# Kernel optimization log

Hardware: AMD Instinct MI355X
Metric: run time of the kernel (lower is better)

The kernel has to match this reference:

```python
import jax, jax.numpy as jnp
import numpy as np

N_NODES = 50000
N_EDGES = 1600000
F_IN = 512      # 2 * embedding_dimension
HID = 512
OUT = 4
NEG_SLOPE = 0.01  # torch LeakyReLU default


def _leaky_relu(x):
    return jnp.where(x >= 0, x, NEG_SLOPE * x)


def setup_inputs() -> dict:
    key = jax.random.key(0)
    ks = jax.random.split(key, 12)
    s_in = 1.0 / np.sqrt(F_IN)
    s_h = 1.0 / np.sqrt(HID)
    return {
        "feature": jax.random.normal(ks[0], (N_NODES, F_IN), jnp.float32),
        "edge_index": jax.random.randint(ks[1], (2, N_EDGES), 0, N_NODES, jnp.int64),
        "edge_type": jax.random.randint(ks[2], (N_EDGES,), 0, 2, jnp.int64),
        # input MLP
        "W_in": jax.random.uniform(ks[3], (F_IN, HID), jnp.float32, -s_in, s_in),
        "b_in": jnp.zeros((HID,), jnp.float32),
        # sage1: lin_l (bias) on aggregated neighbors, lin_r (no bias) on self
        "W1_l": jax.random.uniform(ks[4], (HID, HID), jnp.float32, -s_h, s_h),
        "b1_l": jnp.zeros((HID,), jnp.float32),
        "W1_r": jax.random.uniform(ks[5], (HID, HID), jnp.float32, -s_h, s_h),
        # sage2
        "W2_l": jax.random.uniform(ks[6], (HID, HID), jnp.float32, -s_h, s_h),
        "b2_l": jnp.zeros((HID,), jnp.float32),
        "W2_r": jax.random.uniform(ks[7], (HID, HID), jnp.float32, -s_h, s_h),
        # output linear (hidden -> 4); note forward skips linear_relu_output1
        "W_out": jax.random.uniform(ks[8], (HID, OUT), jnp.float32, -s_h, s_h),
        "b_out": jnp.zeros((OUT,), jnp.float32),
    }


def _sage_conv(x, src, dst, W_l, b_l, W_r):
    # mean aggregation of source features onto destinations (PyG default flow)
    agg = jax.ops.segment_sum(x[src], dst, num_segments=N_NODES)  # [N, H]
    cnt = jax.ops.segment_sum(jnp.ones((src.shape[0], 1), x.dtype), dst,
                              num_segments=N_NODES)               # [N, 1]
    mean = agg / jnp.maximum(cnt, 1.0)
    return mean @ W_l + b_l + x @ W_r


def reference(feature, edge_index, edge_type,
              W_in, b_in, W1_l, b1_l, W1_r, W2_l, b2_l, W2_r, W_out, b_out):
    src, dst = edge_index[0], edge_index[1]
    x = _leaky_relu(feature.astype(jnp.float32) @ W_in + b_in)
    x = _sage_conv(x, src, dst, W1_l, b1_l, W1_r)
    # dropout is identity in eval mode
    x = _sage_conv(x, src, dst, W2_l, b2_l, W2_r)
    return x @ W_out + b_out
```

## Files before the change

kernel.cpp:

```cpp
#include <hip/hip_runtime.h>
#include <stdint.h>

#define NNODES 50000
#define NEDGES 1600000
#define HID 512
#define NEG_SLOPE 0.01f
#define NBUCK 98
#define NBLK 200
#define TILE 8000
#define NSUB 8
#define GPBLK 391
#define MROWS 50048

#define ZTOT4 263040
#define ZBLK 1028
#define TCBLK 1024
#define CABLK 12512
#define SABLK 1025
#define PREP_TC (ZBLK)
#define PREP_CA (ZBLK + TCBLK)
#define PREP_SA (ZBLK + TCBLK + CABLK)
#define PREP_HK (ZBLK + TCBLK + CABLK + SABLK)
#define PREP_GRID (PREP_HK + NBLK)

typedef __attribute__((ext_vector_type(8))) short bf16x8;
typedef __attribute__((ext_vector_type(8))) unsigned short u16x8;
typedef __attribute__((ext_vector_type(4))) float f32x4;

__device__ __forceinline__ unsigned short f2bf(float f) {
  unsigned int u = __builtin_bit_cast(unsigned int, f);
  u += 0x7FFFu + ((u >> 16) & 1u);
  return (unsigned short)(u >> 16);
}
__device__ __forceinline__ void gload_lds16(const void* g, void* l) {
  __builtin_amdgcn_global_load_lds(
      (const __attribute__((address_space(1))) void*)g,
      (__attribute__((address_space(3))) void*)l, 16, 0, 0);
}

__device__ __forceinline__ float wave_dot(const float* __restrict__ Arow,
                                          const float* __restrict__ B, int j) {
  int l = threadIdx.x & 63;
  float4 a0 = *reinterpret_cast<const float4*>(Arow + l * 8);
  float4 a1 = *reinterpret_cast<const float4*>(Arow + l * 8 + 4);
  const float* bb = B + (size_t)(l * 8) * 4 + j;
  float s = a0.x * bb[0] + a0.y * bb[4] + a0.z * bb[8] + a0.w * bb[12] +
            a1.x * bb[16] + a1.y * bb[20] + a1.z * bb[24] + a1.w * bb[28];
#pragma unroll
  for (int off = 1; off < 64; off <<= 1) s += __shfl_xor(s, off);
  return s;
}

__global__ __launch_bounds__(256) void prep(
    const float* __restrict__ feat, const float* __restrict__ W_in,
    const float* __restrict__ W2l, const float* __restrict__ W2r,
    const float* __restrict__ Wout, const float* __restrict__ b2l,
    const float* __restrict__ bout, const int* __restrict__ ei,
    float* __restrict__ zbase, unsigned short* __restrict__ Wt0,
    unsigned short* __restrict__ featb,
    float* __restrict__ Wlp, float* __restrict__ Wrp, float* __restrict__ bp,
    int* __restrict__ hist) {
  __shared__ int h[NBUCK];
  __shared__ int flg;
  int blk = blockIdx.x, t = threadIdx.x;
  if (blk < PREP_TC) {
    int idx = blk * 256 + t;
    if (idx < ZTOT4) reinterpret_cast<float4*>(zbase)[idx] = {0.f, 0.f, 0.f, 0.f};
  } else if (blk < PREP_CA) {
    int i = (blk - PREP_TC) * 256 + t;
    int n = i >> 9, k = i & 511;
    Wt0[i] = f2bf(W_in[(k << 9) | n]);
  } else if (blk < PREP_SA) {
    int idx = (blk - PREP_CA) * 256 + t;
    size_t g = (size_t)idx * 8;
    int row = idx >> 6;
    u16x8 pk;
    if (row < NNODES) {
      float4 v0 = *reinterpret_cast<const float4*>(feat + g);
      float4 v1 = *reinterpret_cast<const float4*>(feat + g + 4);
      pk[0] = f2bf(v0.x); pk[1] = f2bf(v0.y); pk[2] = f2bf(v0.z); pk[3] = f2bf(v0.w);
      pk[4] = f2bf(v1.x); pk[5] = f2bf(v1.y); pk[6] = f2bf(v1.z); pk[7] = f2bf(v1.w);
    } else {
      pk = (u16x8)0;
    }
    *reinterpret_cast<u16x8*>(featb + g) = pk;
  } else if (blk < PREP_HK) {
    int gw = (blk - PREP_SA) * 4 + (t >> 6);
    int l = t & 63;
    if (gw < 2048) {
      float v = wave_dot(W2l + (size_t)(gw >> 2) * 512, Wout, gw & 3);
      if (l == 0) Wlp[gw] = v;
    } else if (gw < 4096) {
      int g = gw - 2048;
      float v = wave_dot(W2r + (size_t)(g >> 2) * 512, Wout, g & 3);
      if (l == 0) Wrp[g] = v;
    } else if (gw < 4100) {
      int j = gw - 4096;
      float v = wave_dot(b2l, Wout, j);
      if (l == 0) bp[j] = v + bout[j];
    }
  } else {
    int hb = blk - PREP_HK;
    for (int i = t; i < NBUCK; i += 256) h[i] = 0;
    if (t < 64) {
      unsigned long long m = __ballot(ei[2 * t + 1] != 0);
      if (t == 0) flg = (m != 0ULL) ? 1 : 0;
    }
    __syncthreads();
    int f = flg;
    int e0 = hb * TILE;
    for (int e = e0 + 2 * t; e < e0 + TILE; e += 512) {
      int d0, d1;
      if (f) {
        int2 v = *reinterpret_cast<const int2*>(&ei[(size_t)NEDGES + e]);
        d0 = v.x; d1 = v.y;
      } else {
        int4 v = *reinterpret_cast<const int4*>(&ei[2 * ((size_t)NEDGES + e)]);
        d0 = v.x; d1 = v.z;
      }
      if ((unsigned)d0 < NNODES) atomicAdd(&h[d0 >> 9], 1);
      if ((unsigned)d1 < NNODES) atomicAdd(&h[d1 >> 9], 1);
    }
    __syncthreads();
    for (int i = t; i < NBUCK; i += 256) hist[i * NBLK + hb] = h[i];
  }
}

__global__ __launch_bounds__(256) void smallB(
    const float* __restrict__ W1l, const float* __restrict__ W1r,
    const float* __restrict__ b1l,
    const float* __restrict__ Wlp, const float* __restrict__ Wrp,
    const float* __restrict__ bp,
    float* __restrict__ Pall, float* __restrict__ kb, float* __restrict__ kc) {
  int gw = blockIdx.x * 4 + (threadIdx.x >> 6);
  int l = threadIdx.x & 63;
  if (gw < 6144) {
    int k = gw / 12, jg = gw % 12;
    int g = jg >> 2, j = jg & 3;
    float v;
    if (g == 0) v = wave_dot(W1l + (size_t)k * 512, Wlp, j);
    else if (g == 1) v = wave_dot(W1r + (size_t)k * 512, Wlp, j) +
                         wave_dot(W1l + (size_t)k * 512, Wrp, j);
    else v = wave_dot(W1r + (size_t)k * 512, Wrp, j);
    if (l == 0) Pall[k * 12 + jg] = v;
  } else if (gw < 6152) {
    int i = gw - 6144, j = i & 3;
    if (i < 4) {
      float v = wave_dot(b1l, Wlp, j);
      if (l == 0) kb[j] = v;
    } else {
      float v = wave_dot(b1l, Wrp, j);
      if (l == 0) kc[j] = v + bp[j];
    }
  }
}

__global__ __launch_bounds__(512) void scanh(int* __restrict__ hist,
                                             int* __restrict__ bstart) {
  __shared__ int s[512];
  const int TOT = NBUCK * NBLK;
  const int C = 40;
  int t = threadIdx.x;
  int base = t * C;
  int sum = 0;
#pragma unroll
  for (int i = 0; i < C; i++) {
    int idx = base + i;
    sum += (idx < TOT) ? hist[idx] : 0;
  }
  s[t] = sum;
  __syncthreads();
  for (int off = 1; off < 512; off <<= 1) {
    int u = (t >= off) ? s[t - off] : 0;
    __syncthreads();
    s[t] += u;
    __syncthreads();
  }
  int run = (t > 0) ? s[t - 1] : 0;
#pragma unroll
  for (int i = 0; i < C; i++) {
    int idx = base + i;
    if (idx < TOT) {
      int v = hist[idx];
      hist[idx] = run;
      if (idx % NBLK == 0) bstart[idx / NBLK] = run;
      run += v;
    }
  }
  if (t == 511) bstart[NBUCK] = s[511];
}

__global__ __launch_bounds__(256) void binscatter(const int* __restrict__ ei,
                                                  const int* __restrict__ hbase,
                                                  unsigned int* __restrict__ pcol) {
  __shared__ unsigned int vals[TILE];
  __shared__ unsigned char bid[TILE];
  __shared__ int lcnt[NBUCK];
  __shared__ int lbase[NBUCK];
  __shared__ int delta[NBUCK];
  __shared__ int flg;
  int t = threadIdx.x, blk = blockIdx.x;
  for (int i = t; i < NBUCK; i += 256) lcnt[i] = 0;
  if (t < 64) {
    unsigned long long m = __ballot(ei[2 * t + 1] != 0);
    if (t == 0) flg = (m != 0ULL) ? 1 : 0;
  }
  __syncthreads();
  int f = flg;
  int e0 = blk * TILE;
  for (int e = e0 + 2 * t; e < e0 + TILE; e += 512) {
    int d0, d1;
    if (f) {
      int2 vd = *reinterpret_cast<const int2*>(&ei[(size_t)NEDGES + e]);
      d0 = vd.x; d1 = vd.y;
    } else {
      int4 vd = *reinterpret_cast<const int4*>(&ei[2 * ((size_t)NEDGES + e)]);
      d0 = vd.x; d1 = vd.z;
    }
    if ((unsigned)d0 < NNODES) atomicAdd(&lcnt[d0 >> 9], 1);
    if ((unsigned)d1 < NNODES) atomicAdd(&lcnt[d1 >> 9], 1);
  }
  __syncthreads();
  if (t == 0) {
    int run = 0;
    for (int b = 0; b < NBUCK; b++) { lbase[b] = run; run += lcnt[b]; }
  }
  __syncthreads();
  for (int b = t; b < NBUCK; b += 256) {
    delta[b] = hbase[b * NBLK + blk] - lbase[b];
    lcnt[b] = 0;
  }
  __syncthreads();
  for (int e = e0 + 2 * t; e < e0 + TILE; e += 512) {
    int s0, s1v, d0, d1;
    if (f) {
      int2 vs = *reinterpret_cast<const int2*>(&ei[e]);
      int2 vd = *reinterpret_cast<const int2*>(&ei[(size_t)NEDGES + e]);
      s0 = vs.x; s1v = vs.y; d0 = vd.x; d1 = vd.y;
    } else {
      int4 vs = *reinterpret_cast<const int4*>(&ei[2 * (size_t)e]);
      int4 vd = *reinterpret_cast<const int4*>(&ei[2 * ((size_t)NEDGES + e)]);
      s0 = vs.x; s1v = vs.z; d0 = vd.x; d1 = vd.z;
    }
    if ((unsigned)d0 < NNODES) {
      if ((unsigned)s0 >= NNODES) s0 = 0;
      int b = d0 >> 9;
      int p = lbase[b] + atomicAdd(&lcnt[b], 1);
      vals[p] = ((unsigned)(d0 & 511) << 16) | (unsigned)s0;
      bid[p] = (unsigned char)b;
    }
    if ((unsigned)d1 < NNODES) {
      if ((unsigned)s1v >= NNODES) s1v = 0;
      int b = d1 >> 9;
      int p = lbase[b] + atomicAdd(&lcnt[b], 1);
      vals[p] = ((unsigned)(d1 & 511) << 16) | (unsigned)s1v;
      bid[p] = (unsigned char)b;
    }
  }
  __syncthreads();
  int total = lbase[NBUCK - 1] + lcnt[NBUCK - 1];
  for (int p = t; p < total; p += 256) {
    pcol[delta[bid[p]] + p] = vals[p];
  }
}

__global__ __launch_bounds__(256, 4) void gemmproj(
    const unsigned short* __restrict__ Ab, const unsigned short* __restrict__ Bt,
    const float* __restrict__ bias, const float* __restrict__ Pall,
    float* __restrict__ t0a, float* __restrict__ t0b, float* __restrict__ t0c) {
  __shared__ unsigned short As[128 * 64];
  __shared__ unsigned short Bs[128 * 64];
  __shared__ float tab[128 * 12];
  const int tid = threadIdx.x;
  const int wave = tid >> 6, lane = tid & 63;
  const int w = blockIdx.x;
  const int mt = (w & 7) + ((w >> 5) << 3);
  const int nb = (w >> 3) & 3;
  if (mt >= GPBLK) return;
  const int bm = mt * 128, bn = nb * 128;
  const int wr = wave >> 1, wc = wave & 1;
  const int r15 = lane & 15, kl = lane >> 4;
  const int srow = lane >> 3;
  const int gslot = (lane & 7) ^ srow;
  const int goff = gslot * 8;

  for (int i = tid; i < 1536; i += 256) tab[i] = 0.f;

  f32x4 acc[4][4];
#pragma unroll
  for (int i = 0; i < 4; i++)
#pragma unroll
    for (int j = 0; j < 4; j++) acc[i][j] = {0.f, 0.f, 0.f, 0.f};

  const int sxa = r15 & 7;

  for (int kt = 0; kt < 8; ++kt) {
#pragma unroll
    for (int q = 0; q < 4; ++q) {
      int c = wave * 4 + q;
      int row = c * 8 + srow;
      gload_lds16(Ab + (size_t)(bm + row) * HID + kt * 64 + goff, (void*)&As[c * 512]);
      gload_lds16(Bt + (size_t)(bn + row) * HID + kt * 64 + goff, (void*)&Bs[c * 512]);
    }
    __syncthreads();
#pragma unroll
    for (int k2 = 0; k2 < 2; ++k2) {
      const int slot = (k2 * 4 + kl) ^ sxa;
      bf16x8 af[4], bfr[4];
#pragma unroll
      for (int mi = 0; mi < 4; ++mi)
        af[mi] = *reinterpret_cast<const bf16x8*>(&As[(wr * 64 + mi * 16 + r15) * 64 + slot * 8]);
#pragma unroll
      for (int ni = 0; ni < 4; ++ni)
        bfr[ni] = *reinterpret_cast<const bf16x8*>(&Bs[(wc * 64 + ni * 16 + r15) * 64 + slot * 8]);
#pragma unroll
      for (int ni = 0; ni < 4; ++ni)
#pragma unroll
        for (int mi = 0; mi < 4; ++mi)
          acc[ni][mi] = __builtin_amdgcn_mfma_f32_16x16x32_bf16(bfr[ni], af[mi], acc[ni][mi], 0, 0, 0);
    }
    __syncthreads();
  }

#pragma unroll
  for (int mi = 0; mi < 4; ++mi) {
    float p12[12];
#pragma unroll
    for (int j = 0; j < 12; ++j) p12[j] = 0.f;
#pragma unroll
    for (int ni = 0; ni < 4; ++ni) {
      int nbase = bn + wc * 64 + ni * 16 + kl * 4;
      float4 bv4 = *reinterpret_cast<const float4*>(bias + nbase);
      float bb[4] = {bv4.x, bv4.y, bv4.z, bv4.w};
#pragma unroll
      for (int rg = 0; rg < 4; ++rg) {
        float v = acc[ni][mi][rg] + bb[rg];
        v = (v >= 0.f) ? v : NEG_SLOPE * v;
        const float* Pc = Pall + (size_t)(nbase + rg) * 12;
        float4 p0 = *reinterpret_cast<const float4*>(Pc);
        float4 p1 = *reinterpret_cast<const float4*>(Pc + 4);
        float4 p2 = *reinterpret_cast<const float4*>(Pc + 8);
        p12[0] += v * p0.x; p12[1] += v * p0.y; p12[2] += v * p0.z; p12[3] += v * p0.w;
        p12[4] += v * p1.x; p12[5] += v * p1.y; p12[6] += v * p1.z; p12[7] += v * p1.w;
        p12[8] += v * p2.x; p12[9] += v * p2.y; p12[10] += v * p2.z; p12[11] += v * p2.w;
      }
    }
#pragma unroll
    for (int j = 0; j < 12; ++j) {
      p12[j] += __shfl_xor(p12[j], 16);
      p12[j] += __shfl_xor(p12[j], 32);
    }
    if (kl == 0) {
      int r = wr * 64 + mi * 16 + r15;
#pragma unroll
      for (int j = 0; j < 12; ++j) atomicAdd(&tab[r * 12 + j], p12[j]);
    }
  }
  __syncthreads();
  for (int i = tid; i < 1536; i += 256) {
    int r = i / 12, j = i - r * 12;
    size_t gr = (size_t)(bm + r);
    float v = tab[i];
    if (j < 4) atomicAdd(&t0a[gr * 4 + j], v);
    else if (j < 8) atomicAdd(&t0b[gr * 4 + (j - 4)], v);
    else atomicAdd(&t0c[gr * 4 + (j - 8)], v);
  }
}

__global__ __launch_bounds__(256) void aggA(
    const unsigned int* __restrict__ pcol, const int* __restrict__ bstart,
    const float* __restrict__ t0a, float* __restrict__ accA) {
  __shared__ float tab[512 * 5];
  int t = threadIdx.x;
  int b = blockIdx.x >> 3, sb = blockIdx.x & 7;
  for (int i = t; i < 2560; i += 256) tab[i] = 0.f;
  __syncthreads();
  int st = bstart[b], en = bstart[b + 1];
  int len = en - st;
  int a0 = st + (int)(((long long)len * sb) >> 3);
  int a1 = st + (int)(((long long)len * (sb + 1)) >> 3);
  for (int e = a0 + t; e < a1; e += 256) {
    unsigned v = pcol[e];
    int i = v >> 16, src = v & 0xFFFF;
    float4 x = *reinterpret_cast<const float4*>(t0a + (size_t)src * 4);
    atomicAdd(&tab[i * 5 + 0], x.x);
    atomicAdd(&tab[i * 5 + 1], x.y);
    atomicAdd(&tab[i * 5 + 2], x.z);
    atomicAdd(&tab[i * 5 + 3], x.w);
    atomicAdd(&tab[i * 5 + 4], 1.f);
  }
  __syncthreads();
  float* o = accA + (size_t)b * 2560;
  for (int i = t; i < 2560; i += 256) {
    float v = tab[i];
    if (v != 0.f) atomicAdd(&o[i], v);
  }
}

__global__ __launch_bounds__(256) void finA(
    const float* __restrict__ accA, const float* __restrict__ t0b,
    float* __restrict__ s1, float* __restrict__ degf) {
  int n = blockIdx.x * 256 + threadIdx.x;
  if (n >= NNODES) return;
  const float* a = accA + (size_t)n * 5;
  float deg = a[4];
  float sc = (deg > 0.f) ? 1.f / deg : 0.f;
  float4 tb = *reinterpret_cast<const float4*>(t0b + (size_t)n * 4);
  float4 o = {a[0] * sc + tb.x, a[1] * sc + tb.y, a[2] * sc + tb.z, a[3] * sc + tb.w};
  *reinterpret_cast<float4*>(s1 + (size_t)n * 4) = o;
  degf[n] = deg;
}

__global__ __launch_bounds__(256) void aggB(
    const unsigned int* __restrict__ pcol, const int* __restrict__ bstart,
    const float* __restrict__ s1, float* __restrict__ accB) {
  __shared__ float tab[512 * 4];
  int t = threadIdx.x;
  int b = blockIdx.x >> 3, sb = blockIdx.x & 7;
  for (int i = t; i < 2048; i += 256) tab[i] = 0.f;
  __syncthreads();
  int st = bstart[b], en = bstart[b + 1];
  int len = en - st;
  int a0 = st + (int)(((long long)len * sb) >> 3);
  int a1 = st + (int)(((long long)len * (sb + 1)) >> 3);
  for (int e = a0 + t; e < a1; e += 256) {
    unsigned v = pcol[e];
    int i = v >> 16, src = v & 0xFFFF;
    float4 x = *reinterpret_cast<const float4*>(s1 + (size_t)src * 4);
    atomicAdd(&tab[i * 4 + 0], x.x);
    atomicAdd(&tab[i * 4 + 1], x.y);
    atomicAdd(&tab[i * 4 + 2], x.z);
    atomicAdd(&tab[i * 4 + 3], x.w);
  }
  __syncthreads();
  float* o = accB + (size_t)b * 2048;
  for (int i = t; i < 2048; i += 256) {
    float v = tab[i];
    if (v != 0.f) atomicAdd(&o[i], v);
  }
}

__global__ __launch_bounds__(256) void finB(
    const float* __restrict__ accB, const float* __restrict__ t0c,
    const float* __restrict__ degf, const float* __restrict__ kb,
    const float* __restrict__ kc, float* __restrict__ out) {
  int n = blockIdx.x * 256 + threadIdx.x;
  if (n >= NNODES) return;
  const float* a = accB + (size_t)n * 4;
  float deg = degf[n];
  float sc = (deg > 0.f) ? 1.f / deg : 0.f;
  float ind = (deg > 0.f) ? 1.f : 0.f;
  float4 c = *reinterpret_cast<const float4*>(t0c + (size_t)n * 4);
  float4 vb = *reinterpret_cast<const float4*>(kb);
  float4 vc = *reinterpret_cast<const float4*>(kc);
  float4 o = {a[0] * sc + c.x + ind * vb.x + vc.x,
              a[1] * sc + c.y + ind * vb.y + vc.y,
              a[2] * sc + c.z + ind * vb.z + vc.z,
              a[3] * sc + c.w + ind * vb.w + vc.w};
  *reinterpret_cast<float4*>(out + (size_t)n * 4) = o;
}

extern "C" void kernel_launch(void* const* d_in, const int* in_sizes, int n_in,
                              void* d_out, int out_size, void* d_ws, size_t ws_size,
                              hipStream_t stream) {
  const float* feat = (const float*)d_in[0];
  const int* ei = (const int*)d_in[1];
  const float* W_in = (const float*)d_in[3];
  const float* b_in = (const float*)d_in[4];
  const float* W1l = (const float*)d_in[5];
  const float* b1l = (const float*)d_in[6];
  const float* W1r = (const float*)d_in[7];
  const float* W2l = (const float*)d_in[8];
  const float* b2l = (const float*)d_in[9];
  const float* W2r = (const float*)d_in[10];
  const float* Wout = (const float*)d_in[11];
  const float* bout = (const float*)d_in[12];
  float* out = (float*)d_out;

  char* ws = (char*)d_ws;
  size_t off = 0;
  auto alloc = [&](size_t bytes) {
    void* p = ws + off;
    off += (bytes + 15) & ~(size_t)15;
    return p;
  };
  float* t0a  = (float*)alloc((size_t)MROWS * 4 * 4);
  float* t0b  = (float*)alloc((size_t)MROWS * 4 * 4);
  float* t0c  = (float*)alloc((size_t)MROWS * 4 * 4);
  float* accA = (float*)alloc((size_t)NBUCK * 2560 * 4);
  float* accB = (float*)alloc((size_t)NBUCK * 2048 * 4);
  float* zbase = t0a;

  int* hist   = (int*)alloc((size_t)NBUCK * NBLK * 4);
  int* bstart = (int*)alloc((NBUCK + 1) * 4);
  unsigned int* pcol = (unsigned int*)alloc((size_t)NEDGES * 4);
  unsigned short* featb = (unsigned short*)alloc((size_t)MROWS * HID * 2);
  unsigned short* Wt0 = (unsigned short*)alloc(512 * 512 * 2);
  float* Wlp  = (float*)alloc(2048 * 4);
  float* Wrp  = (float*)alloc(2048 * 4);
  float* bp   = (float*)alloc(16);
  float* Pall = (float*)alloc(512 * 12 * 4);
  float* kb   = (float*)alloc(16);
  float* kc   = (float*)alloc(16);
  float* s1   = (float*)alloc((size_t)MROWS * 4 * 4);
  float* degf = (float*)alloc((size_t)NNODES * 4);
  (void)ws_size;

  prep<<<PREP_GRID, 256, 0, stream>>>(feat, W_in, W2l, W2r, Wout, b2l, bout, ei,
                                      zbase, Wt0, featb, Wlp, Wrp, bp, hist);
  smallB<<<1538, 256, 0, stream>>>(W1l, W1r, b1l, Wlp, Wrp, bp, Pall, kb, kc);

  scanh<<<1, 512, 0, stream>>>(hist, bstart);
  binscatter<<<NBLK, 256, 0, stream>>>(ei, hist, pcol);

  gemmproj<<<1568, 256, 0, stream>>>(featb, Wt0, b_in, Pall, t0a, t0b, t0c);
  aggA<<<NBUCK * NSUB, 256, 0, stream>>>(pcol, bstart, t0a, accA);
  finA<<<(NNODES + 255) / 256, 256, 0, stream>>>(accA, t0b, s1, degf);
  aggB<<<NBUCK * NSUB, 256, 0, stream>>>(pcol, bstart, s1, accB);
  finB<<<(NNODES + 255) / 256, 256, 0, stream>>>(accB, t0c, degf, kb, kc, out);
}
```

Baseline: 299.2 us.

## Replace global atomics with per-block partial buffers and deterministic reduction passes

Global atomic accumulation in gemmproj, aggA and aggB is replaced by plain stores into per-block partial buffers. A new reduce_t0 kernel and extended finA/finB sum those partials, which also removes the zero-initialisation blocks from prep. gemmproj is retiled to 128x64 output tiles with a 32-wide K step, giving 8 column blocks and a larger grid. The cost is extra workspace traffic, an additional kernel launch, and a smaller K tile with more barriers per GEMM.

```diff
diff --git a/kernel.cpp b/kernel.cpp
--- a/kernel.cpp
+++ b/kernel.cpp
@@ -11,16 +11,14 @@
 #define NSUB 8
 #define GPBLK 391
 #define MROWS 50048
-
-#define ZTOT4 263040
-#define ZBLK 1028
+#define NNB 8
+
 #define TCBLK 1024
 #define CABLK 12512
 #define SABLK 1025
-#define PREP_TC (ZBLK)
-#define PREP_CA (ZBLK + TCBLK)
-#define PREP_SA (ZBLK + TCBLK + CABLK)
-#define PREP_HK (ZBLK + TCBLK + CABLK + SABLK)
+#define PREP_CA (TCBLK)
+#define PREP_SA (TCBLK + CABLK)
+#define PREP_HK (TCBLK + CABLK + SABLK)
 #define PREP_GRID (PREP_HK + NBLK)
 
 typedef __attribute__((ext_vector_type(8))) short bf16x8;
@@ -56,18 +54,14 @@
     const float* __restrict__ W2l, const float* __restrict__ W2r,
     const float* __restrict__ Wout, const float* __restrict__ b2l,
     const float* __restrict__ bout, const int* __restrict__ ei,
-    float* __restrict__ zbase, unsigned short* __restrict__ Wt0,
-    unsigned short* __restrict__ featb,
+    unsigned short* __restrict__ Wt0, unsigned short* __restrict__ featb,
     float* __restrict__ Wlp, float* __restrict__ Wrp, float* __restrict__ bp,
     int* __restrict__ hist) {
   __shared__ int h[NBUCK];
   __shared__ int flg;
   int blk = blockIdx.x, t = threadIdx.x;
-  if (blk < PREP_TC) {
-    int idx = blk * 256 + t;
-    if (idx < ZTOT4) reinterpret_cast<float4*>(zbase)[idx] = {0.f, 0.f, 0.f, 0.f};
-  } else if (blk < PREP_CA) {
-    int i = (blk - PREP_TC) * 256 + t;
+  if (blk < PREP_CA) {
+    int i = blk * 256 + t;
     int n = i >> 9, k = i & 511;
     Wt0[i] = f2bf(W_in[(k << 9) | n]);
   } else if (blk < PREP_SA) {
@@ -267,58 +261,53 @@
 __global__ __launch_bounds__(256, 4) void gemmproj(
     const unsigned short* __restrict__ Ab, const unsigned short* __restrict__ Bt,
     const float* __restrict__ bias, const float* __restrict__ Pall,
-    float* __restrict__ t0a, float* __restrict__ t0b, float* __restrict__ t0c) {
-  __shared__ unsigned short As[128 * 64];
-  __shared__ unsigned short Bs[128 * 64];
-  __shared__ float tab[128 * 12];
+    float* __restrict__ t0p) {
+  __shared__ unsigned short As[128 * 32];
+  __shared__ unsigned short Bs[64 * 32];
+  __shared__ float tab[2][128 * 12];
   const int tid = threadIdx.x;
   const int wave = tid >> 6, lane = tid & 63;
   const int w = blockIdx.x;
-  const int mt = (w & 7) + ((w >> 5) << 3);
-  const int nb = (w >> 3) & 3;
+  const int mt = (w & 7) + ((w >> 6) << 3);
+  const int nb = (w >> 3) & 7;
   if (mt >= GPBLK) return;
-  const int bm = mt * 128, bn = nb * 128;
+  const int bm = mt * 128, bn = nb * 64;
   const int wr = wave >> 1, wc = wave & 1;
   const int r15 = lane & 15, kl = lane >> 4;
-  const int srow = lane >> 3;
-  const int gslot = (lane & 7) ^ srow;
-  const int goff = gslot * 8;
-
-  for (int i = tid; i < 1536; i += 256) tab[i] = 0.f;
-
-  f32x4 acc[4][4];
-#pragma unroll
-  for (int i = 0; i < 4; i++)
+  const int srow = lane >> 2, soff = (lane & 3) * 8;
+
+  for (int i = tid; i < 1536; i += 256) { tab[0][i] = 0.f; tab[1][i] = 0.f; }
+
+  f32x4 acc[2][4];
+#pragma unroll
+  for (int i = 0; i < 2; i++)
 #pragma unroll
     for (int j = 0; j < 4; j++) acc[i][j] = {0.f, 0.f, 0.f, 0.f};
 
-  const int sxa = r15 & 7;
-
-  for (int kt = 0; kt < 8; ++kt) {
-#pragma unroll
-    for (int q = 0; q < 4; ++q) {
-      int c = wave * 4 + q;
-      int row = c * 8 + srow;
-      gload_lds16(Ab + (size_t)(bm + row) * HID + kt * 64 + goff, (void*)&As[c * 512]);
-      gload_lds16(Bt + (size_t)(bn + row) * HID + kt * 64 + goff, (void*)&Bs[c * 512]);
+  for (int kt = 0; kt < HID / 32; ++kt) {
+#pragma unroll
+    for (int rr = 0; rr < 2; ++rr) {
+      int c = wave * 2 + rr;
+      int row = c * 16 + srow;
+      gload_lds16(Ab + (size_t)(bm + row) * HID + kt * 32 + soff, (void*)&As[c * 512]);
+    }
+    {
+      int row = wave * 16 + srow;
+      gload_lds16(Bt + (size_t)(bn + row) * HID + kt * 32 + soff, (void*)&Bs[wave * 512]);
     }
     __syncthreads();
-#pragma unroll
-    for (int k2 = 0; k2 < 2; ++k2) {
-      const int slot = (k2 * 4 + kl) ^ sxa;
-      bf16x8 af[4], bfr[4];
+    bf16x8 af[4], bfr[2];
+#pragma unroll
+    for (int mi = 0; mi < 4; ++mi)
+      af[mi] = *reinterpret_cast<const bf16x8*>(&As[(wr * 64 + mi * 16 + r15) * 32 + kl * 8]);
+#pragma unroll
+    for (int ni = 0; ni < 2; ++ni)
+      bfr[ni] = *reinterpret_cast<const bf16x8*>(&Bs[(wc * 32 + ni * 16 + r15) * 32 + kl * 8]);
+#pragma unroll
+    for (int ni = 0; ni < 2; ++ni)
 #pragma unroll
       for (int mi = 0; mi < 4; ++mi)
-        af[mi] = *reinterpret_cast<const bf16x8*>(&As[(wr * 64 + mi * 16 + r15) * 64 + slot * 8]);
-#pragma unroll
-      for (int ni = 0; ni < 4; ++ni)
-        bfr[ni] = *reinterpret_cast<const bf16x8*>(&Bs[(wc * 64 + ni * 16 + r15) * 64 + slot * 8]);
-#pragma unroll
-      for (int ni = 0; ni < 4; ++ni)
-#pragma unroll
-        for (int mi = 0; mi < 4; ++mi)
-          acc[ni][mi] = __builtin_amdgcn_mfma_f32_16x16x32_bf16(bfr[ni], af[mi], acc[ni][mi], 0, 0, 0);
-    }
+        acc[ni][mi] = __builtin_amdgcn_mfma_f32_16x16x32_bf16(bfr[ni], af[mi], acc[ni][mi], 0, 0, 0);
     __syncthreads();
   }
 
@@ -328,8 +317,8 @@
 #pragma unroll
     for (int j = 0; j < 12; ++j) p12[j] = 0.f;
 #pragma unroll
-    for (int ni = 0; ni < 4; ++ni) {
-      int nbase = bn + wc * 64 + ni * 16 + kl * 4;
+    for (int ni = 0; ni < 2; ++ni) {
+      int nbase = bn + wc * 32 + ni * 16 + kl * 4;
       float4 bv4 = *reinterpret_cast<const float4*>(bias + nbase);
       float bb[4] = {bv4.x, bv4.y, bv4.z, bv4.w};
 #pragma unroll
@@ -353,23 +342,40 @@
     if (kl == 0) {
       int r = wr * 64 + mi * 16 + r15;
 #pragma unroll
-      for (int j = 0; j < 12; ++j) atomicAdd(&tab[r * 12 + j], p12[j]);
-    }
-  }
-  __syncthreads();
-  for (int i = tid; i < 1536; i += 256) {
-    int r = i / 12, j = i - r * 12;
-    size_t gr = (size_t)(bm + r);
-    float v = tab[i];
-    if (j < 4) atomicAdd(&t0a[gr * 4 + j], v);
-    else if (j < 8) atomicAdd(&t0b[gr * 4 + (j - 4)], v);
-    else atomicAdd(&t0c[gr * 4 + (j - 8)], v);
-  }
+      for (int j = 0; j < 12; ++j) tab[wc][r * 12 + j] = p12[j];
+    }
+  }
+  __syncthreads();
+  float* o = t0p + ((size_t)nb * MROWS + bm) * 12;
+  for (int i = tid; i < 1536; i += 256) o[i] = tab[0][i] + tab[1][i];
+}
+
+__global__ __launch_bounds__(256) void reduce_t0(
+    const float* __restrict__ t0p, float* __restrict__ t0a,
+    float* __restrict__ t0b, float* __restrict__ t0c) {
+  int n = blockIdx.x * 256 + threadIdx.x;
+  if (n >= NNODES) return;
+  float s[12];
+#pragma unroll
+  for (int j = 0; j < 12; ++j) s[j] = 0.f;
+#pragma unroll
+  for (int p = 0; p < NNB; ++p) {
+    const float* q = t0p + ((size_t)p * MROWS + n) * 12;
+    float4 a = *reinterpret_cast<const float4*>(q);
+    float4 b = *reinterpret_cast<const float4*>(q + 4);
+    float4 c = *reinterpret_cast<const float4*>(q + 8);
+    s[0] += a.x; s[1] += a.y; s[2] += a.z; s[3] += a.w;
+    s[4] += b.x; s[5] += b.y; s[6] += b.z; s[7] += b.w;
+    s[8] += c.x; s[9] += c.y; s[10] += c.z; s[11] += c.w;
+  }
+  *reinterpret_cast<float4*>(t0a + (size_t)n * 4) = {s[0], s[1], s[2], s[3]};
+  *reinterpret_cast<float4*>(t0b + (size_t)n * 4) = {s[4], s[5], s[6], s[7]};
+  *reinterpret_cast<float4*>(t0c + (size_t)n * 4) = {s[8], s[9], s[10], s[11]};
 }
 
 __global__ __launch_bounds__(256) void aggA(
     const unsigned int* __restrict__ pcol, const int* __restrict__ bstart,
-    const float* __restrict__ t0a, float* __restrict__ accA) {
+    const float* __restrict__ t0a, float* __restrict__ partialA) {
   __shared__ float tab[512 * 5];
   int t = threadIdx.x;
   int b = blockIdx.x >> 3, sb = blockIdx.x & 7;
@@ -390,19 +396,23 @@
     atomicAdd(&tab[i * 5 + 4], 1.f);
   }
   __syncthreads();
-  float* o = accA + (size_t)b * 2560;
-  for (int i = t; i < 2560; i += 256) {
-    float v = tab[i];
-    if (v != 0.f) atomicAdd(&o[i], v);
-  }
+  float* o = partialA + (size_t)blockIdx.x * 2560;
+  for (int i = t; i < 2560; i += 256) o[i] = tab[i];
 }
 
 __global__ __launch_bounds__(256) void finA(
-    const float* __restrict__ accA, const float* __restrict__ t0b,
+    const float* __restrict__ partialA, const float* __restrict__ t0b,
     float* __restrict__ s1, float* __restrict__ degf) {
   int n = blockIdx.x * 256 + threadIdx.x;
   if (n >= NNODES) return;
-  const float* a = accA + (size_t)n * 5;
+  int b = n >> 9, i = n & 511;
+  float a[5] = {0.f, 0.f, 0.f, 0.f, 0.f};
+#pragma unroll
+  for (int s = 0; s < 8; s++) {
+    const float* p = partialA + (size_t)(b * 8 + s) * 2560 + i * 5;
+#pragma unroll
+    for (int j = 0; j < 5; j++) a[j] += p[j];
+  }
   float deg = a[4];
   float sc = (deg > 0.f) ? 1.f / deg : 0.f;
   float4 tb = *reinterpret_cast<const float4*>(t0b + (size_t)n * 4);
@@ -413,7 +423,7 @@
 
 __global__ __launch_bounds__(256) void aggB(
     const unsigned int* __restrict__ pcol, const int* __restrict__ bstart,
-    const float* __restrict__ s1, float* __restrict__ accB) {
+    const float* __restrict__ s1, float* __restrict__ partialB) {
   __shared__ float tab[512 * 4];
   int t = threadIdx.x;
   int b = blockIdx.x >> 3, sb = blockIdx.x & 7;
@@ -433,20 +443,24 @@
     atomicAdd(&tab[i * 4 + 3], x.w);
   }
   __syncthreads();
-  float* o = accB + (size_t)b * 2048;
-  for (int i = t; i < 2048; i += 256) {
-    float v = tab[i];
-    if (v != 0.f) atomicAdd(&o[i], v);
-  }
+  float* o = partialB + (size_t)blockIdx.x * 2048;
+  for (int i = t; i < 2048; i += 256) o[i] = tab[i];
 }
 
 __global__ __launch_bounds__(256) void finB(
-    const float* __restrict__ accB, const float* __restrict__ t0c,
+    const float* __restrict__ partialB, const float* __restrict__ t0c,
     const float* __restrict__ degf, const float* __restrict__ kb,
     const float* __restrict__ kc, float* __restrict__ out) {
   int n = blockIdx.x * 256 + threadIdx.x;
   if (n >= NNODES) return;
-  const float* a = accB + (size_t)n * 4;
+  int b = n >> 9, i = n & 511;
+  float a[4] = {0.f, 0.f, 0.f, 0.f};
+#pragma unroll
+  for (int s = 0; s < 8; s++) {
+    const float* p = partialB + (size_t)(b * 8 + s) * 2048 + i * 4;
+#pragma unroll
+    for (int j = 0; j < 4; j++) a[j] += p[j];
+  }
   float deg = degf[n];
   float sc = (deg > 0.f) ? 1.f / deg : 0.f;
   float ind = (deg > 0.f) ? 1.f : 0.f;
@@ -487,10 +501,9 @@
   float* t0a  = (float*)alloc((size_t)MROWS * 4 * 4);
   float* t0b  = (float*)alloc((size_t)MROWS * 4 * 4);
   float* t0c  = (float*)alloc((size_t)MROWS * 4 * 4);
-  float* accA = (float*)alloc((size_t)NBUCK * 2560 * 4);
-  float* accB = (float*)alloc((size_t)NBUCK * 2048 * 4);
-  float* zbase = t0a;
-
+  float* partialA = (float*)alloc((size_t)NBUCK * NSUB * 2560 * 4);
+  float* partialB = (float*)alloc((size_t)NBUCK * NSUB * 2048 * 4);
+  float* t0p  = (float*)alloc((size_t)NNB * MROWS * 12 * 4);
   int* hist   = (int*)alloc((size_t)NBUCK * NBLK * 4);
   int* bstart = (int*)alloc((NBUCK + 1) * 4);
   unsigned int* pcol = (unsigned int*)alloc((size_t)NEDGES * 4);
@@ -507,15 +520,16 @@
   (void)ws_size;
 
   prep<<<PREP_GRID, 256, 0, stream>>>(feat, W_in, W2l, W2r, Wout, b2l, bout, ei,
-                                      zbase, Wt0, featb, Wlp, Wrp, bp, hist);
+                                      Wt0, featb, Wlp, Wrp, bp, hist);
   smallB<<<1538, 256, 0, stream>>>(W1l, W1r, b1l, Wlp, Wrp, bp, Pall, kb, kc);
 
   scanh<<<1, 512, 0, stream>>>(hist, bstart);
   binscatter<<<NBLK, 256, 0, stream>>>(ei, hist, pcol);
 
-  gemmproj<<<1568, 256, 0, stream>>>(featb, Wt0, b_in, Pall, t0a, t0b, t0c);
-  aggA<<<NBUCK * NSUB, 256, 0, stream>>>(pcol, bstart, t0a, accA);
-  finA<<<(NNODES + 255) / 256, 256, 0, stream>>>(accA, t0b, s1, degf);
-  aggB<<<NBUCK * NSUB, 256, 0, stream>>>(pcol, bstart, s1, accB);
-  finB<<<(NNODES + 255) / 256, 256, 0, stream>>>(accB, t0c, degf, kb, kc, out);
-}
+  gemmproj<<<49 * 64, 256, 0, stream>>>(featb, Wt0, b_in, Pall, t0p);
+  reduce_t0<<<(NNODES + 255) / 256, 256, 0, stream>>>(t0p, t0a, t0b, t0c);
+  aggA<<<NBUCK * NSUB, 256, 0, stream>>>(pcol, bstart, t0a, partialA);
+  finA<<<(NNODES + 255) / 256, 256, 0, stream>>>(partialA, t0b, s1, degf);
+  aggB<<<NBUCK * NSUB, 256, 0, stream>>>(pcol, bstart, s1, partialB);
+  finB<<<(NNODES + 255) / 256, 256, 0, stream>>>(partialB, t0c, degf, kb, kc, out);
+}
```

New measurement: 301.2 us. About the same (+0.7%).
